# Kernel optimization log

Hardware: AMD Instinct MI355X
Metric: run time of the kernel (lower is better)

The kernel has to match this reference:

```python
import jax, jax.numpy as jnp
import numpy as np

TOP_K = 2  # matches init kwarg top_k


def setup_inputs() -> dict:
    key = jax.random.key(0)
    k1, k2, k3, k4 = jax.random.split(key, 4)
    B, S, D, E = 4, 2048, 1024, 8
    x = jax.random.normal(k1, (B, S, D), dtype=jnp.float32)
    w_gate = jax.random.normal(k2, (D, E), dtype=jnp.float32) * 0.02
    w1 = jax.random.normal(k3, (E, D, 4 * D), dtype=jnp.float32) * 0.02
    w2 = jax.random.normal(k4, (E, 4 * D, D), dtype=jnp.float32) * 0.02
    return {"x": x, "w_gate": w_gate, "w1": w1, "w2": w2}


def reference(x, w_gate, w1, w2):
    # x: [B, S, D]; w_gate: [D, E]; w1: [E, D, 4D]; w2: [E, 4D, D]
    B, S, D = x.shape
    E = w1.shape[0]
    xt = x.reshape(-1, D)                      # [T, D], T = B*S
    T = xt.shape[0]

    logits = xt @ w_gate                       # [T, E]
    topk_vals, topk_idx = jax.lax.top_k(logits, TOP_K)  # [T, K]
    gates = jax.nn.softmax(topk_vals, axis=-1)          # [T, K]

    # Combine weights per (token, expert): scatter the top-k gates.
    comb = jnp.zeros((T, E), dtype=x.dtype)
    comb = comb.at[jnp.arange(T)[:, None], topk_idx].add(gates)  # [T, E]

    # Dense per-expert FFN over all tokens, masked by combine weight.
    # (Loop over the small fixed expert count; each iteration is a big GEMM.)
    out = jnp.zeros_like(xt)
    for e in range(E):
        h = jax.nn.relu(xt @ w1[e])            # [T, 4D]
        y = h @ w2[e]                          # [T, D]
        out = out + comb[:, e:e + 1] * y
    return out.reshape(B, S, D)
```

## Files before the change

### kernel.cpp

```cpp
#include <hip/hip_runtime.h>
#include <hip/hip_bf16.h>


#define T_TOK   8192
#define DIM     1024
#define NEXP    8
#define HID     4096

typedef unsigned short ushort_t;
typedef __attribute__((ext_vector_type(8))) short bfrag;
typedef __attribute__((ext_vector_type(4))) float f32x4;

__device__ __forceinline__ ushort_t f2bf(float f) {
    union { float f; unsigned int u; } v; v.f = f;
    unsigned int r = v.u + 0x7FFFu + ((v.u >> 16) & 1u);
    return (ushort_t)(r >> 16);
}

__device__ __forceinline__ void async_load16(const void* g, void* l) {
    __builtin_amdgcn_global_load_lds(
        (const __attribute__((address_space(1))) unsigned int*)g,
        (__attribute__((address_space(3))) unsigned int*)l, 16, 0, 0);
}

__global__ __launch_bounds__(256)
void route_kern(const float* __restrict__ x, const float* __restrict__ wg,
                ushort_t* __restrict__ x_bf, int* __restrict__ topk,
                float* __restrict__ gates, int* __restrict__ counts)
{
    const int w = threadIdx.x >> 6, lane = threadIdx.x & 63;
    const int t = blockIdx.x * 4 + w;
    const float* xr = x + (size_t)t * DIM;
    float acc[8];
#pragma unroll
    for (int e = 0; e < 8; ++e) acc[e] = 0.f;

#pragma unroll
    for (int it = 0; it < 4; ++it) {
        const int j = it * 256 + lane * 4;
        float4 xv = *(const float4*)(xr + j);
        ushort4 xb;
        xb.x = f2bf(xv.x); xb.y = f2bf(xv.y); xb.z = f2bf(xv.z); xb.w = f2bf(xv.w);
        *(ushort4*)(x_bf + (size_t)t * DIM + j) = xb;
        const float xs[4] = {xv.x, xv.y, xv.z, xv.w};
#pragma unroll
        for (int jj = 0; jj < 4; ++jj) {
            float4 g0 = *(const float4*)(wg + (size_t)(j + jj) * 8);
            float4 g1 = *(const float4*)(wg + (size_t)(j + jj) * 8 + 4);
            acc[0] += xs[jj] * g0.x; acc[1] += xs[jj] * g0.y;
            acc[2] += xs[jj] * g0.z; acc[3] += xs[jj] * g0.w;
            acc[4] += xs[jj] * g1.x; acc[5] += xs[jj] * g1.y;
            acc[6] += xs[jj] * g1.z; acc[7] += xs[jj] * g1.w;
        }
    }
#pragma unroll
    for (int d = 1; d < 64; d <<= 1)
#pragma unroll
        for (int e = 0; e < 8; ++e) acc[e] += __shfl_xor(acc[e], d);

    if (lane == 0) {
        int i0 = 0; float v0 = acc[0];
#pragma unroll
        for (int e = 1; e < 8; ++e) if (acc[e] > v0) { v0 = acc[e]; i0 = e; }
        int i1 = -1; float v1 = -1e30f;
#pragma unroll
        for (int e = 0; e < 8; ++e) if (e != i0 && acc[e] > v1) { v1 = acc[e]; i1 = e; }
        float ex = __expf(v1 - v0);
        float inv = 1.f / (1.f + ex);
        topk[t * 2] = i0; topk[t * 2 + 1] = i1;
        gates[t * 2] = inv; gates[t * 2 + 1] = ex * inv;
        atomicAdd(&counts[i0], 1);
        atomicAdd(&counts[i1], 1);
    }
}

__global__ void scan_kern(const int* __restrict__ counts, int* __restrict__ offs,
                          int* __restrict__ cursors)
{
    if (threadIdx.x == 0) {
        int o = 0;
        for (int e = 0; e < NEXP; ++e) { offs[e] = o; cursors[e] = o; o += counts[e]; }
        offs[NEXP] = o;
    }
}

__global__ __launch_bounds__(256)
void scatter_kern(const int* __restrict__ topk, const float* __restrict__ gates,
                  int* __restrict__ cursors, int* __restrict__ tok_c,
                  float* __restrict__ gate_c)
{
    const int t = blockIdx.x * 256 + threadIdx.x;
#pragma unroll
    for (int k = 0; k < 2; ++k) {
        int e = topk[t * 2 + k];
        int pos = atomicAdd(&cursors[e], 1);
        tok_c[pos] = t;
        gate_c[pos] = gates[t * 2 + k];
    }
}

__global__ __launch_bounds__(256)
void transp_kern(const float* __restrict__ in, ushort_t* __restrict__ out, int K, int N)
{
    __shared__ float tile[64][65];
    const int e = blockIdx.z;
    const size_t ibase = (size_t)e * K * N, obase = (size_t)e * N * K;
    const int k0 = blockIdx.y * 64, n0 = blockIdx.x * 64;
    const int tid = threadIdx.x;

    const int r = tid >> 4, c4 = (tid & 15) * 4;
#pragma unroll
    for (int p = 0; p < 4; ++p) {
        int kk = p * 16 + r;
        float4 v = *(const float4*)(in + ibase + (size_t)(k0 + kk) * N + n0 + c4);
        tile[kk][c4] = v.x; tile[kk][c4 + 1] = v.y; tile[kk][c4 + 2] = v.z; tile[kk][c4 + 3] = v.w;
    }
    __syncthreads();
    const int k8 = (tid & 7) * 8, nr = tid >> 3;
#pragma unroll
    for (int p = 0; p < 2; ++p) {
        int nn = p * 32 + nr;
        bfrag v;
#pragma unroll
        for (int j = 0; j < 8; ++j) v[j] = (short)f2bf(tile[k8 + j][nn]);
        *(bfrag*)(out + obase + (size_t)(n0 + nn) * K + k0 + k8) = v;
    }
}

template <int STAGE, int NTK, int NBF, int SPLITK, int KF, int NF>
__global__ __launch_bounds__(256)
void gemm_kern(const ushort_t* __restrict__ A, const ushort_t* __restrict__ Bt,
               ushort_t* __restrict__ Hout, float* __restrict__ Out,
               const int* __restrict__ eoff, const int* __restrict__ tok_c,
               const float* __restrict__ gate_c)
{
    constexpr int MBF = 64;
    __shared__ ushort_t ldsA[128 * 64];
    __shared__ ushort_t ldsB[128 * 64];

    constexpr int nb = NEXP * MBF * NBF;
    const int orig = blockIdx.x;
    const int lg = (orig & 7) * (nb >> 3) + (orig >> 3);
    const int e = lg / (MBF * NBF);
    const int rem = lg - e * (MBF * NBF);
    const int mblk = rem / NBF;
    const int nidx = rem - mblk * NBF;
    const int nblk = nidx / SPLITK;
    const int ks = nidx - nblk * SPLITK;
    const int kbeg = ks * NTK * 64;

    const int base = eoff[e];
    const int cnt = eoff[e + 1] - base;
    const int m0 = mblk * 128;
    if (m0 >= cnt) return;
    const int n0 = nblk * 128;

    const int tid = threadIdx.x;
    const int w = tid >> 6, lane = tid & 63;
    const int lhi = lane >> 4, llo = lane & 15;

    const ushort_t* asrc[4];
    const ushort_t* bsrc[4];
    int ldsoff[4];
    const ushort_t* Bbase = Bt + (size_t)e * (size_t)NF * (size_t)KF;
#pragma unroll
    for (int i = 0; i < 4; ++i) {
        int ci = ((i * 4 + w) << 6) + lane;
        int r = ci >> 3;
        int cb = (ci & 7) << 4;
        int sb = cb ^ ((r & 7) << 4);
        int gr = m0 + r; if (gr >= cnt) gr = cnt - 1;
        size_t arow = (STAGE == 1) ? (size_t)tok_c[base + gr] * (size_t)KF
                                   : (size_t)(base + gr) * (size_t)KF;
        asrc[i] = A + arow + (sb >> 1);
        bsrc[i] = Bbase + (size_t)(n0 + r) * KF + (sb >> 1);
        ldsoff[i] = (i * 4 + w) << 10;
    }

    f32x4 acc[4][4];
#pragma unroll
    for (int m = 0; m < 4; ++m)
#pragma unroll
        for (int n = 0; n < 4; ++n) acc[m][n] = (f32x4)(0.f);

    const int wr = (w >> 1) << 6;
    const int wc = (w & 1) << 6;

    for (int kt = 0; kt < NTK; ++kt) {
        const int k0 = kbeg + kt * 64;
#pragma unroll
        for (int i = 0; i < 4; ++i) {
            async_load16(asrc[i] + k0, (char*)ldsA + ldsoff[i]);
            async_load16(bsrc[i] + k0, (char*)ldsB + ldsoff[i]);
        }
        __syncthreads();
#pragma unroll
        for (int s = 0; s < 2; ++s) {
            bfrag a[4], b[4];
            const int kb = (s << 6) + (lhi << 4);
#pragma unroll
            for (int m = 0; m < 4; ++m) {
                int row = wr + (m << 4) + llo;
                a[m] = *(const bfrag*)((const char*)ldsA + row * 128 + (kb ^ ((row & 7) << 4)));
            }
#pragma unroll
            for (int n = 0; n < 4; ++n) {
                int row = wc + (n << 4) + llo;
                b[n] = *(const bfrag*)((const char*)ldsB + row * 128 + (kb ^ ((row & 7) << 4)));
            }
#pragma unroll
            for (int m = 0; m < 4; ++m)
#pragma unroll
                for (int n = 0; n < 4; ++n)
                    acc[m][n] = __builtin_amdgcn_mfma_f32_16x16x32_bf16(a[m], b[n], acc[m][n], 0, 0, 0);
        }
        __syncthreads();
    }

    if (STAGE == 1) {
#pragma unroll
        for (int m = 0; m < 4; ++m)
#pragma unroll
            for (int i = 0; i < 4; ++i) {
                int row = wr + (m << 4) + (lhi << 2) + i;
                int gr = m0 + row;
                if (gr >= cnt) continue;
                size_t rb = (size_t)(base + gr) * (size_t)NF + n0 + wc;
#pragma unroll
                for (int n = 0; n < 4; ++n) {
                    float v = acc[m][n][i];
                    Hout[rb + (n << 4) + llo] = f2bf(v > 0.f ? v : 0.f);
                }
            }
    } else {
#pragma unroll
        for (int m = 0; m < 4; ++m)
#pragma unroll
            for (int i = 0; i < 4; ++i) {
                int row = wr + (m << 4) + (lhi << 2) + i;
                int gr = m0 + row;
                if (gr >= cnt) continue;
                int tok = tok_c[base + gr];
                float g = gate_c[base + gr];
                size_t rb = (size_t)tok * (size_t)NF + n0 + wc;
#pragma unroll
                for (int n = 0; n < 4; ++n)
                    atomicAdd(&Out[rb + (n << 4) + llo], g * acc[m][n][i]);
            }
    }
}

extern "C" void kernel_launch(void* const* d_in, const int* in_sizes, int n_in,
                              void* d_out, int out_size, void* d_ws, size_t ws_size,
                              hipStream_t stream)
{
    const float* x  = (const float*)d_in[0];
    const float* wg = (const float*)d_in[1];
    const float* w1 = (const float*)d_in[2];
    const float* w2 = (const float*)d_in[3];
    float* out = (float*)d_out;

    char* ws = (char*)d_ws;
    ushort_t* x_bf = (ushort_t*)(ws + 0);
    ushort_t* w1t  = (ushort_t*)(ws + 16777216);
    ushort_t* w2t  = (ushort_t*)(ws + 83886080);
    ushort_t* h    = (ushort_t*)(ws + 150994944);
    char* ctrl     = ws + 285212672;
    int*   topk    = (int*)(ctrl);
    float* gates   = (float*)(ctrl + 65536);
    int*   tok_c   = (int*)(ctrl + 131072);
    float* gate_c  = (float*)(ctrl + 196608);
    int*   counts  = (int*)(ctrl + 262144);
    int*   offs    = (int*)(ctrl + 262144 + 64);
    int*   cursors = (int*)(ctrl + 262144 + 128);

    hipMemsetAsync(counts, 0, NEXP * sizeof(int), stream);
    hipMemsetAsync(out, 0, (size_t)T_TOK * DIM * sizeof(float), stream);

    route_kern<<<T_TOK / 4, 256, 0, stream>>>(x, wg, x_bf, topk, gates, counts);
    transp_kern<<<dim3(HID / 64, DIM / 64, NEXP), 256, 0, stream>>>(w1, w1t, DIM, HID);
    transp_kern<<<dim3(DIM / 64, HID / 64, NEXP), 256, 0, stream>>>(w2, w2t, HID, DIM);
    scan_kern<<<1, 64, 0, stream>>>(counts, offs, cursors);
    scatter_kern<<<T_TOK / 256, 256, 0, stream>>>(topk, gates, cursors, tok_c, gate_c);

    gemm_kern<1, 16, 32, 1, 1024, 4096><<<NEXP * 64 * 32, 256, 0, stream>>>(
        x_bf, w1t, h, nullptr, offs, tok_c, gate_c);
    gemm_kern<2, 32, 16, 2, 4096, 1024><<<NEXP * 64 * 16, 256, 0, stream>>>(
        h, w2t, nullptr, out, offs, tok_c, gate_c);
}
```

Baseline: 883.0 us.

## Remap GEMM blocks so each XCD shares A rows and drop split-K in stage 2

Block indices are remapped so consecutive blocks on the same XCD handle every N tile of one (expert, M-block) row group. The A tile is then reused out of that XCD's L2 rather than being spread across chips. Stage 2 no longer splits K in two: each block walks the full 4096 reduction, which halves the atomicAdd traffic into the output at the cost of fewer, longer blocks. Variables were renamed to avoid shadowing.

```diff
diff --git a/kernel.cpp b/kernel.cpp
--- a/kernel.cpp
+++ b/kernel.cpp
@@ -127,33 +127,30 @@
     }
 }
 
-template <int STAGE, int NTK, int NBF, int SPLITK, int KF, int NF>
+template <int STAGE, int NTK, int NBLK, int KF, int NF>
 __global__ __launch_bounds__(256)
 void gemm_kern(const ushort_t* __restrict__ A, const ushort_t* __restrict__ Bt,
                ushort_t* __restrict__ Hout, float* __restrict__ Out,
                const int* __restrict__ eoff, const int* __restrict__ tok_c,
                const float* __restrict__ gate_c)
 {
-    constexpr int MBF = 64;
     __shared__ ushort_t ldsA[128 * 64];
     __shared__ ushort_t ldsB[128 * 64];
 
-    constexpr int nb = NEXP * MBF * NBF;
-    const int orig = blockIdx.x;
-    const int lg = (orig & 7) * (nb >> 3) + (orig >> 3);
-    const int e = lg / (MBF * NBF);
-    const int rem = lg - e * (MBF * NBF);
-    const int mblk = rem / NBF;
-    const int nidx = rem - mblk * NBF;
-    const int nblk = nidx / SPLITK;
-    const int ks = nidx - nblk * SPLITK;
-    const int kbeg = ks * NTK * 64;
+    constexpr int LN = (NBLK == 32) ? 5 : 3;
+    const int b = blockIdx.x;
+    const int xcd = b & 7;
+    const int n = (b >> 3) & (NBLK - 1);
+    const int u = b >> (3 + LN);
+    const int g = xcd + (u << 3);
+    const int e = g >> 6;
+    const int mblk = g & 63;
 
     const int base = eoff[e];
     const int cnt = eoff[e + 1] - base;
     const int m0 = mblk * 128;
     if (m0 >= cnt) return;
-    const int n0 = nblk * 128;
+    const int n0 = n * 128;
 
     const int tid = threadIdx.x;
     const int w = tid >> 6, lane = tid & 63;
@@ -181,13 +178,13 @@
 #pragma unroll
     for (int m = 0; m < 4; ++m)
 #pragma unroll
-        for (int n = 0; n < 4; ++n) acc[m][n] = (f32x4)(0.f);
+        for (int nn = 0; nn < 4; ++nn) acc[m][nn] = (f32x4)(0.f);
 
     const int wr = (w >> 1) << 6;
     const int wc = (w & 1) << 6;
 
     for (int kt = 0; kt < NTK; ++kt) {
-        const int k0 = kbeg + kt * 64;
+        const int k0 = kt * 64;
 #pragma unroll
         for (int i = 0; i < 4; ++i) {
             async_load16(asrc[i] + k0, (char*)ldsA + ldsoff[i]);
@@ -196,7 +193,7 @@
         __syncthreads();
 #pragma unroll
         for (int s = 0; s < 2; ++s) {
-            bfrag a[4], b[4];
+            bfrag a[4], bb[4];
             const int kb = (s << 6) + (lhi << 4);
 #pragma unroll
             for (int m = 0; m < 4; ++m) {
@@ -204,15 +201,15 @@
                 a[m] = *(const bfrag*)((const char*)ldsA + row * 128 + (kb ^ ((row & 7) << 4)));
             }
 #pragma unroll
-            for (int n = 0; n < 4; ++n) {
-                int row = wc + (n << 4) + llo;
-                b[n] = *(const bfrag*)((const char*)ldsB + row * 128 + (kb ^ ((row & 7) << 4)));
+            for (int nn = 0; nn < 4; ++nn) {
+                int row = wc + (nn << 4) + llo;
+                bb[nn] = *(const bfrag*)((const char*)ldsB + row * 128 + (kb ^ ((row & 7) << 4)));
             }
 #pragma unroll
             for (int m = 0; m < 4; ++m)
 #pragma unroll
-                for (int n = 0; n < 4; ++n)
-                    acc[m][n] = __builtin_amdgcn_mfma_f32_16x16x32_bf16(a[m], b[n], acc[m][n], 0, 0, 0);
+                for (int nn = 0; nn < 4; ++nn)
+                    acc[m][nn] = __builtin_amdgcn_mfma_f32_16x16x32_bf16(a[m], bb[nn], acc[m][nn], 0, 0, 0);
         }
         __syncthreads();
     }
@@ -227,9 +224,9 @@
                 if (gr >= cnt) continue;
                 size_t rb = (size_t)(base + gr) * (size_t)NF + n0 + wc;
 #pragma unroll
-                for (int n = 0; n < 4; ++n) {
-                    float v = acc[m][n][i];
-                    Hout[rb + (n << 4) + llo] = f2bf(v > 0.f ? v : 0.f);
+                for (int nn = 0; nn < 4; ++nn) {
+                    float v = acc[m][nn][i];
+                    Hout[rb + (nn << 4) + llo] = f2bf(v > 0.f ? v : 0.f);
                 }
             }
     } else {
@@ -241,11 +238,11 @@
                 int gr = m0 + row;
                 if (gr >= cnt) continue;
                 int tok = tok_c[base + gr];
-                float g = gate_c[base + gr];
+                float gg = gate_c[base + gr];
                 size_t rb = (size_t)tok * (size_t)NF + n0 + wc;
 #pragma unroll
-                for (int n = 0; n < 4; ++n)
-                    atomicAdd(&Out[rb + (n << 4) + llo], g * acc[m][n][i]);
+                for (int nn = 0; nn < 4; ++nn)
+                    atomicAdd(&Out[rb + (nn << 4) + llo], gg * acc[m][nn][i]);
             }
     }
 }
@@ -283,8 +280,8 @@
     scan_kern<<<1, 64, 0, stream>>>(counts, offs, cursors);
     scatter_kern<<<T_TOK / 256, 256, 0, stream>>>(topk, gates, cursors, tok_c, gate_c);
 
-    gemm_kern<1, 16, 32, 1, 1024, 4096><<<NEXP * 64 * 32, 256, 0, stream>>>(
+    gemm_kern<1, 16, 32, 1024, 4096><<<16384, 256, 0, stream>>>(
         x_bf, w1t, h, nullptr, offs, tok_c, gate_c);
-    gemm_kern<2, 32, 16, 2, 4096, 1024><<<NEXP * 64 * 16, 256, 0, stream>>>(
+    gemm_kern<2, 64, 8, 4096, 1024><<<4096, 256, 0, stream>>>(
         h, w2t, nullptr, out, offs, tok_c, gate_c);
 }
```

New measurement: 923.0 us. 1.05x slower.
